# Kernel tuning notes

Measured on AMD Instinct MI355X. Metric: run time of the kernel, lower is better.

The kernel has to match this reference:

```python
import jax, jax.numpy as jnp
import numpy as np

N = 50000   # nodes
E = 800000  # edges
D = 128     # node_channels


def setup_inputs() -> dict:
    key = jax.random.key(0)
    ks = jax.random.split(key, 16)
    s = 1.0 / np.sqrt(D)
    inp = {
        "x": jax.random.normal(ks[0], (N, D), dtype=jnp.float32),
        "edge_index": jax.random.randint(ks[1], (2, E), 0, N, dtype=jnp.int64),
        "eps": jax.random.normal(ks[2], (N, D), dtype=jnp.float32),
    }
    names = ["1", "2", "mu", "logstd", "5", "6"]
    for i, nm in enumerate(names):
        inp[f"W{nm}"] = jax.random.normal(ks[3 + 2 * i], (D, D), dtype=jnp.float32) * s
        inp[f"b{nm}"] = jnp.zeros((D,), dtype=jnp.float32)
    return inp


def _gcn_norm(edge_index, num_nodes):
    # add self-loops, then symmetric normalization deg^{-1/2} (A+I) deg^{-1/2}
    loop = jnp.arange(num_nodes, dtype=edge_index.dtype)
    src = jnp.concatenate([edge_index[0], loop])
    dst = jnp.concatenate([edge_index[1], loop])
    deg = jax.ops.segment_sum(jnp.ones_like(src, dtype=jnp.float32), dst,
                              num_segments=num_nodes)
    dis = jnp.where(deg > 0, jax.lax.rsqrt(deg), 0.0)
    norm = dis[src] * dis[dst]  # [E + N]
    return src, dst, norm


def _gcn(x, W, b, src, dst, norm, num_nodes):
    h = x @ W                              # [N, D] small GEMM
    msg = h[src] * norm[:, None]           # gather + scale, [E+N, D]
    out = jax.ops.segment_sum(msg, dst, num_segments=num_nodes)  # scatter-add
    return out + b


def reference(x, edge_index, eps, W1, b1, W2, b2, Wmu, bmu, Wlogstd, blogstd,
              W5, b5, W6, b6):
    num_nodes = x.shape[0]
    src, dst, norm = _gcn_norm(edge_index, num_nodes)
    g = lambda h, W, b: _gcn(h, W, b, src, dst, norm, num_nodes)

    nodes = jax.nn.relu(g(x, W1, b1))
    nodes = jax.nn.relu(g(nodes, W2, b2))
    mu = g(nodes, Wmu, bmu)
    logstd = g(nodes, Wlogstd, blogstd)
    # reparametrize (training mode), divider = 10
    nodes = mu + eps * jnp.exp(logstd) / 10.0
    nodes = jax.nn.relu(g(nodes, W5, b5))
    nodes = jax.nn.relu(g(nodes, W6, b6))
    return nodes
```

## Files before the change

kernel.cpp:

```cpp
#include <hip/hip_runtime.h>
#include <hip/hip_bf16.h>
#include <cstdint>
#include <cstddef>

#define D 128
#define NWG 200

typedef _Float16 f16;
typedef f16 f16x2 __attribute__((ext_vector_type(2)));
typedef f16 f16x4 __attribute__((ext_vector_type(4)));
typedef f16 f16x8 __attribute__((ext_vector_type(8)));
typedef float f32x4 __attribute__((ext_vector_type(4)));

static inline size_t align256(size_t x){ return (x + 255) & ~(size_t)255; }

__global__ void detect_kernel(const int* __restrict__ ei, long long n32, int* __restrict__ flag){
  __shared__ int s;
  if (threadIdx.x == 0) s = 0;
  __syncthreads();
  int nz = 0;
  for (long long i = 2LL*threadIdx.x + 1; i < 4096 && i < n32; i += 512)
    nz |= (ei[i] != 0);
  if (nz) s = 1;
  __syncthreads();
  if (threadIdx.x == 0) *flag = (s ? 0 : 1);
}

__device__ __forceinline__ void load_edge(const void* ei, int E, int is64, int e, int& s, int& d){
  if (is64) {
    const long long* p = (const long long*)ei;
    s = (int)p[e]; d = (int)p[(size_t)E + e];
  } else {
    const int* p = (const int*)ei;
    s = p[e]; d = p[(size_t)E + e];
  }
}

__global__ __launch_bounds__(256) void passA_hist(
    const void* __restrict__ ei, int E, const int* __restrict__ flag,
    int* __restrict__ glob_hist, int NB){
  __shared__ int cnt[256];
  int t = threadIdx.x, wg = blockIdx.x;
  cnt[t] = 0;
  __syncthreads();
  int is64 = *flag;
  int chunk = (E + NWG - 1) / NWG;
  int lo = wg * chunk, hi = min(lo + chunk, E);
  for (int e = lo + t; e < hi; e += 256){
    int s, d;
    load_edge(ei, E, is64, e, s, d);
    atomicAdd(&cnt[d >> 8], 1);
  }
  __syncthreads();
  for (int b = t; b < NB; b += 256)
    glob_hist[b * NWG + wg] = cnt[b];
}

__global__ void scan_partial(const int* __restrict__ src, int* __restrict__ dst,
                             int* __restrict__ blockSums, int L){
  __shared__ int sd[256];
  int t = threadIdx.x;
  int base = blockIdx.x * 1024 + t * 4;
  int v[4]; int s = 0;
  #pragma unroll
  for (int j = 0; j < 4; ++j){ v[j] = (base + j < L) ? src[base + j] : 0; s += v[j]; }
  sd[t] = s; __syncthreads();
  for (int off = 1; off < 256; off <<= 1){
    int x = (t >= off) ? sd[t - off] : 0;
    __syncthreads();
    sd[t] += x;
    __syncthreads();
  }
  int run = sd[t] - s;
  #pragma unroll
  for (int j = 0; j < 4; ++j){
    if (base + j < L) dst[base + j] = run;
    run += v[j];
  }
  if (t == 255) blockSums[blockIdx.x] = sd[255];
}

__global__ void scan_blocksums(int* __restrict__ blockSums, int nblk,
                               int* __restrict__ dst, int L, int total){
  __shared__ int sd[256];
  int t = threadIdx.x;
  int v = (t < nblk) ? blockSums[t] : 0;
  sd[t] = v; __syncthreads();
  for (int off = 1; off < 256; off <<= 1){
    int x = (t >= off) ? sd[t - off] : 0;
    __syncthreads();
    sd[t] += x;
    __syncthreads();
  }
  if (t < nblk) blockSums[t] = sd[t] - v;
  if (t == 0) dst[L] = total;
}

__global__ void scan_add(int* __restrict__ dst, const int* __restrict__ blockSums, int L){
  int i = blockIdx.x * blockDim.x + threadIdx.x;
  if (i >= L) return;
  dst[i] += blockSums[i >> 10];
}

__global__ __launch_bounds__(256) void passB_scatter(
    const void* __restrict__ ei, int E, const int* __restrict__ flag,
    const int* __restrict__ bucketOff, int NB, unsigned* __restrict__ packed){
  __shared__ int cur[256];
  int t = threadIdx.x, wg = blockIdx.x;
  for (int b = t; b < NB; b += 256)
    cur[b] = bucketOff[b * NWG + wg];
  __syncthreads();
  int is64 = *flag;
  int chunk = (E + NWG - 1) / NWG;
  int lo = wg * chunk, hi = min(lo + chunk, E);
  for (int e = lo + t; e < hi; e += 256){
    int s, d;
    load_edge(ei, E, is64, e, s, d);
    int pos = atomicAdd(&cur[d >> 8], 1);
    packed[pos] = (unsigned)s | ((unsigned)(d & 255) << 16);
  }
}

__global__ __launch_bounds__(256) void passC_csr(
    const unsigned* __restrict__ packed, const int* __restrict__ bucketOff,
    int NB, int N, int E,
    int* __restrict__ rowptr, float* __restrict__ dis, int* __restrict__ csr_src){
  __shared__ int degl[256];
  __shared__ int sd[256];
  __shared__ int cur[256];
  int t = threadIdx.x, b = blockIdx.x;
  int begin = bucketOff[(size_t)b * NWG];
  int endb  = bucketOff[(size_t)(b + 1) * NWG];
  degl[t] = 0;
  __syncthreads();
  for (int i = begin + t; i < endb; i += 256)
    atomicAdd(&degl[(packed[i] >> 16) & 255], 1);
  __syncthreads();
  int dv = degl[t];
  sd[t] = dv; __syncthreads();
  for (int off = 1; off < 256; off <<= 1){
    int x = (t >= off) ? sd[t - off] : 0;
    __syncthreads();
    sd[t] += x;
    __syncthreads();
  }
  int localOff = sd[t] - dv;
  int v = b * 256 + t;
  if (v < N){
    rowptr[v] = begin + localOff;
    dis[v] = rsqrtf((float)(dv + 1));
  }
  if (b == NB - 1 && t == 0) rowptr[N] = E;
  cur[t] = begin + localOff;
  __syncthreads();
  for (int i = begin + t; i < endb; i += 256){
    unsigned p = packed[i];
    int pos = atomicAdd(&cur[(p >> 16) & 255], 1);
    csr_src[pos] = (int)(p & 0xFFFFu);
  }
}

__global__ void cast_scale(const float* __restrict__ in, const float* __restrict__ dis,
                           f16* __restrict__ out, int n4){
  int i = blockIdx.x * blockDim.x + threadIdx.x;
  if (i >= n4) return;
  float dv = dis[i >> 5];
  float4 v = ((const float4*)in)[i];
  f16x4 o; o[0]=(f16)(v.x*dv); o[1]=(f16)(v.y*dv); o[2]=(f16)(v.z*dv); o[3]=(f16)(v.w*dv);
  ((f16x4*)out)[i] = o;
}

__global__ void prep_w(const float* __restrict__ Wa, const float* __restrict__ Wb,
                       const float* __restrict__ Wc, const float* __restrict__ Wd,
                       const float* __restrict__ We, const float* __restrict__ Wf,
                       f16* __restrict__ Wt){
  int i = blockIdx.x * 256 + threadIdx.x;
  int w = i >> 14, rem = i & 16383;
  int n = rem >> 7, k = rem & 127;
  const float* Wp = (w==0)?Wa:(w==1)?Wb:(w==2)?Wc:(w==3)?Wd:(w==4)?We:Wf;
  Wt[i] = (f16)Wp[k*128 + n];
}

__global__ __launch_bounds__(256) void agg16(
    const f16* __restrict__ in, f16* __restrict__ out,
    const int* __restrict__ rowptr, const int* __restrict__ csr_src,
    const float* __restrict__ dis, int N){
  int v = blockIdx.x * 4 + (threadIdx.x >> 6);
  if (v >= N) return;
  int c2 = (threadIdx.x & 63) * 2;
  float dv = dis[v];
  int beg = rowptr[v], end = rowptr[v + 1];
  f16x2 sv = *(const f16x2*)&in[(size_t)v * D + c2];
  float acc0 = (float)sv[0], acc1 = (float)sv[1];
  int e = beg;
  for (; e + 7 < end; e += 8){
    f16x2 h[8];
    #pragma unroll
    for (int j = 0; j < 8; ++j){
      int u = csr_src[e + j];
      h[j] = *(const f16x2*)&in[(size_t)u * D + c2];
    }
    #pragma unroll
    for (int j = 0; j < 8; ++j){ acc0 += (float)h[j][0]; acc1 += (float)h[j][1]; }
  }
  for (; e + 1 < end; e += 2){
    int u0 = csr_src[e], u1 = csr_src[e + 1];
    f16x2 h0 = *(const f16x2*)&in[(size_t)u0 * D + c2];
    f16x2 h1 = *(const f16x2*)&in[(size_t)u1 * D + c2];
    acc0 += (float)h0[0] + (float)h1[0];
    acc1 += (float)h0[1] + (float)h1[1];
  }
  if (e < end){
    int u = csr_src[e];
    f16x2 h = *(const f16x2*)&in[(size_t)u * D + c2];
    acc0 += (float)h[0]; acc1 += (float)h[1];
  }
  f16x2 o; o[0] = (f16)(acc0 * dv); o[1] = (f16)(acc1 * dv);
  *(f16x2*)&out[(size_t)v * D + c2] = o;
}

template<int EPI>
__global__ __launch_bounds__(512) void gemm_mfma(
    const f16* __restrict__ A, const f16* __restrict__ Wt, const float* __restrict__ bias,
    const f16* __restrict__ Wt2, const float* __restrict__ bias2,
    const float* __restrict__ eps, const float* __restrict__ dis,
    f16* __restrict__ out16, float* __restrict__ outf, int N){

  extern __shared__ __align__(16) f16 Ws[];

  int t = threadIdx.x;
  int wave = t >> 6, lane = t & 63;
  int lrow = lane & 15, hi = lane >> 4;
  int r0 = blockIdx.x * 128 + wave * 16;
  bool active = (r0 < N);

  f16x8 a[4];
  if (active){
    int rr = min(r0 + lrow, N - 1);
    const f16* arow = &A[(size_t)rr * D + hi * 8];
    #pragma unroll
    for (int s = 0; s < 4; ++s) a[s] = *(const f16x8*)&arow[s * 32];
  }

  {
    int r = t & 127, p = t >> 7;
    const float4* src = (const float4*)&Wt[r * 128 + p * 32];
    f16* dstrow = &Ws[r * 128];
    #pragma unroll
    for (int i = 0; i < 4; ++i){
      int q = p * 4 + i;
      *(float4*)&dstrow[(q ^ (r & 7)) * 8] = src[i];
    }
    if (EPI == 1){
      const float4* src2 = (const float4*)&Wt2[r * 128 + p * 32];
      f16* dstrow2 = &Ws[16384 + r * 128];
      #pragma unroll
      for (int i = 0; i < 4; ++i){
        int q = p * 4 + i;
        *(float4*)&dstrow2[(q ^ (r & 7)) * 8] = src2[i];
      }
    }
  }
  __syncthreads();
  if (!active) return;

  f32x4 acc[8] = {};
  f32x4 acc2[8] = {};

  #pragma unroll
  for (int s = 0; s < 4; ++s){
    #pragma unroll
    for (int tt = 0; tt < 8; ++tt){
      int n = tt * 16 + lrow;
      int q = (s * 4 + hi) ^ (lrow & 7);
      f16x8 b = *(const f16x8*)&Ws[n * 128 + q * 8];
      acc[tt] = __builtin_amdgcn_mfma_f32_16x16x32_f16(b, a[s], acc[tt], 0, 0, 0);
      if (EPI == 1){
        f16x8 b2 = *(const f16x8*)&Ws[16384 + n * 128 + q * 8];
        acc2[tt] = __builtin_amdgcn_mfma_f32_16x16x32_f16(b2, a[s], acc2[tt], 0, 0, 0);
      }
    }
  }

  int r = r0 + lrow;
  if (r >= N) return;
  float dv = (EPI == 2) ? 1.f : dis[r];
  int cbase = hi * 4;
  #pragma unroll
  for (int tt = 0; tt < 8; ++tt){
    int n0 = tt * 16 + cbase;
    f32x4 bv = *(const f32x4*)&bias[n0];
    if (EPI == 0){
      f16x4 o;
      #pragma unroll
      for (int ii = 0; ii < 4; ++ii)
        o[ii] = (f16)(fmaxf(acc[tt][ii] + bv[ii], 0.f) * dv);
      *(f16x4*)&out16[(size_t)r * D + n0] = o;
    } else if (EPI == 1){
      f32x4 bv2 = *(const f32x4*)&bias2[n0];
      f32x4 e4  = *(const f32x4*)&eps[(size_t)r * D + n0];
      f16x4 o;
      #pragma unroll
      for (int ii = 0; ii < 4; ++ii){
        float mu = acc[tt][ii] + bv[ii];
        float ls = acc2[tt][ii] + bv2[ii];
        o[ii] = (f16)((mu + e4[ii] * __expf(ls) * 0.1f) * dv);
      }
      *(f16x4*)&out16[(size_t)r * D + n0] = o;
    } else {
      f32x4 o;
      #pragma unroll
      for (int ii = 0; ii < 4; ++ii)
        o[ii] = fmaxf(acc[tt][ii] + bv[ii], 0.f);
      *(f32x4*)&outf[(size_t)r * D + n0] = o;
    }
  }
}

extern "C" void kernel_launch(void* const* d_in, const int* in_sizes, int n_in,
                              void* d_out, int out_size, void* d_ws, size_t ws_size,
                              hipStream_t stream){
  const float* x   = (const float*)d_in[0];
  const void*  ei  = d_in[1];
  const float* eps = (const float*)d_in[2];
  const float* W1  = (const float*)d_in[3];  const float* b1  = (const float*)d_in[4];
  const float* W2  = (const float*)d_in[5];  const float* b2  = (const float*)d_in[6];
  const float* Wmu = (const float*)d_in[7];  const float* bmu = (const float*)d_in[8];
  const float* Wls = (const float*)d_in[9];  const float* bls = (const float*)d_in[10];
  const float* W5  = (const float*)d_in[11]; const float* b5  = (const float*)d_in[12];
  const float* W6  = (const float*)d_in[13]; const float* b6  = (const float*)d_in[14];

  const int N = in_sizes[0] / D;
  const int E = in_sizes[1] / 2;
  const int NB = (N + 255) >> 8;
  const int L  = NB * NWG;
  float* out = (float*)d_out;

  char* ws = (char*)d_ws;
  size_t off = 0;
  auto alloc = [&](size_t bytes){ char* p = ws + off; off += align256(bytes); return p; };
  int*      flag      = (int*)     alloc(256);
  int*      glob_hist = (int*)     alloc(((size_t)L + 1) * 4);
  int*      bucketOff = (int*)     alloc(((size_t)L + 1) * 4);
  int*      blockSums = (int*)     alloc(1024);
  int*      rowptr    = (int*)     alloc(((size_t)N + 1) * 4);
  float*    dis       = (float*)   alloc((size_t)N * 4);
  unsigned* packed    = (unsigned*)alloc((size_t)E * 4);
  int*      csr_src   = (int*)     alloc((size_t)E * 4);
  f16*      Wt        = (f16*)     alloc((size_t)6 * 128 * 128 * 2);
  f16*      bufA      = (f16*)     alloc((size_t)N * D * 2);
  f16*      bufB      = (f16*)     alloc((size_t)N * D * 2);
  (void)ws_size; (void)n_in; (void)out_size;

  detect_kernel<<<1, 256, 0, stream>>>((const int*)ei, (long long)2 * E, flag);

  passA_hist<<<NWG, 256, 0, stream>>>(ei, E, flag, glob_hist, NB);
  int nblk = (L + 1023) / 1024;
  scan_partial<<<nblk, 256, 0, stream>>>(glob_hist, bucketOff, blockSums, L);
  scan_blocksums<<<1, 256, 0, stream>>>(blockSums, nblk, bucketOff, L, E);
  scan_add<<<(L + 255) / 256, 256, 0, stream>>>(bucketOff, blockSums, L);
  passB_scatter<<<NWG, 256, 0, stream>>>(ei, E, flag, bucketOff, NB, packed);
  passC_csr<<<NB, 256, 0, stream>>>(packed, bucketOff, NB, N, E, rowptr, dis, csr_src);

  cast_scale<<<(N * D / 4 + 255) / 256, 256, 0, stream>>>(x, dis, bufB, N * D / 4);
  prep_w<<<(6 * 16384) / 256, 256, 0, stream>>>(W1, W2, Wmu, Wls, W5, W6, Wt);

  int aggGrid = (N + 3) / 4;
  int gemmGrid = (N + 127) / 128;
  size_t lds1 = 128 * 128 * sizeof(f16);
  size_t lds2 = 2 * 128 * 128 * sizeof(f16);

  agg16<<<aggGrid, 256, 0, stream>>>(bufB, bufA, rowptr, csr_src, dis, N);
  gemm_mfma<0><<<gemmGrid, 512, lds1, stream>>>(bufA, Wt + 0*16384, b1, nullptr, nullptr, nullptr, dis, bufB, nullptr, N);
  agg16<<<aggGrid, 256, 0, stream>>>(bufB, bufA, rowptr, csr_src, dis, N);
  gemm_mfma<0><<<gemmGrid, 512, lds1, stream>>>(bufA, Wt + 1*16384, b2, nullptr, nullptr, nullptr, dis, bufB, nullptr, N);
  agg16<<<aggGrid, 256, 0, stream>>>(bufB, bufA, rowptr, csr_src, dis, N);
  gemm_mfma<1><<<gemmGrid, 512, lds2, stream>>>(bufA, Wt + 2*16384, bmu, Wt + 3*16384, bls, eps, dis, bufB, nullptr, N);
  agg16<<<aggGrid, 256, 0, stream>>>(bufB, bufA, rowptr, csr_src, dis, N);
  gemm_mfma<0><<<gemmGrid, 512, lds1, stream>>>(bufA, Wt + 4*16384, b5, nullptr, nullptr, nullptr, dis, bufB, nullptr, N);
  agg16<<<aggGrid, 256, 0, stream>>>(bufB, bufA, rowptr, csr_src, dis, N);
  gemm_mfma<2><<<gemmGrid, 512, lds1, stream>>>(bufA, Wt + 5*16384, b6, nullptr, nullptr, nullptr, dis, nullptr, out, N);
}
```

Baseline: 396.6 us.

## Slice aggregation over feature columns and store CSR sources as 16-bit

The gather-aggregate kernel is split into four column passes of 32 channels each. Every node's 64-lane wave now processes four edges at once (16 lanes per edge) and combines the partial sums with cross-lane shuffles. Each pass touches a 64-byte slice of the feature rows, so its working set is a quarter of the node table, which is meant to improve L2/MALL hit rates on random gathers. CSR source indices are stored as u16 to halve index traffic, and index loads and output stores use nontemporal hints. The cost is four times as many blocks and four re-reads of the index arrays.

```diff
diff --git a/kernel.cpp b/kernel.cpp
--- a/kernel.cpp
+++ b/kernel.cpp
@@ -11,6 +11,7 @@
 typedef f16 f16x4 __attribute__((ext_vector_type(4)));
 typedef f16 f16x8 __attribute__((ext_vector_type(8)));
 typedef float f32x4 __attribute__((ext_vector_type(4)));
+typedef unsigned short u16;
 
 static inline size_t align256(size_t x){ return (x + 255) & ~(size_t)255; }
 
@@ -124,7 +125,7 @@
 __global__ __launch_bounds__(256) void passC_csr(
     const unsigned* __restrict__ packed, const int* __restrict__ bucketOff,
     int NB, int N, int E,
-    int* __restrict__ rowptr, float* __restrict__ dis, int* __restrict__ csr_src){
+    int* __restrict__ rowptr, float* __restrict__ dis, u16* __restrict__ csr_src){
   __shared__ int degl[256];
   __shared__ int sd[256];
   __shared__ int cur[256];
@@ -156,7 +157,7 @@
   for (int i = begin + t; i < endb; i += 256){
     unsigned p = packed[i];
     int pos = atomicAdd(&cur[(p >> 16) & 255], 1);
-    csr_src[pos] = (int)(p & 0xFFFFu);
+    csr_src[pos] = (u16)(p & 0xFFFFu);
   }
 }
 
@@ -181,42 +182,48 @@
   Wt[i] = (f16)Wp[k*128 + n];
 }
 
-__global__ __launch_bounds__(256) void agg16(
+__global__ __launch_bounds__(256) void agg_sliced(
     const f16* __restrict__ in, f16* __restrict__ out,
-    const int* __restrict__ rowptr, const int* __restrict__ csr_src,
-    const float* __restrict__ dis, int N){
-  int v = blockIdx.x * 4 + (threadIdx.x >> 6);
+    const int* __restrict__ rowptr, const u16* __restrict__ csr_src,
+    const float* __restrict__ dis, int N, int nodeBlocks){
+  int bid = blockIdx.x;
+  int pass = bid / nodeBlocks;
+  int nb   = bid - pass * nodeBlocks;
+  int v = nb * 4 + (threadIdx.x >> 6);
   if (v >= N) return;
-  int c2 = (threadIdx.x & 63) * 2;
-  float dv = dis[v];
+  int lane = threadIdx.x & 63;
+  int q  = lane >> 4;
+  int sl = lane & 15;
+  int c0 = pass * 32 + sl * 2;
+  const f16* base = in + c0;
+
   int beg = rowptr[v], end = rowptr[v + 1];
-  f16x2 sv = *(const f16x2*)&in[(size_t)v * D + c2];
-  float acc0 = (float)sv[0], acc1 = (float)sv[1];
-  int e = beg;
-  for (; e + 7 < end; e += 8){
-    f16x2 h[8];
-    #pragma unroll
-    for (int j = 0; j < 8; ++j){
-      int u = csr_src[e + j];
-      h[j] = *(const f16x2*)&in[(size_t)u * D + c2];
-    }
-    #pragma unroll
-    for (int j = 0; j < 8; ++j){ acc0 += (float)h[j][0]; acc1 += (float)h[j][1]; }
-  }
-  for (; e + 1 < end; e += 2){
-    int u0 = csr_src[e], u1 = csr_src[e + 1];
-    f16x2 h0 = *(const f16x2*)&in[(size_t)u0 * D + c2];
-    f16x2 h1 = *(const f16x2*)&in[(size_t)u1 * D + c2];
+  float acc0 = 0.f, acc1 = 0.f;
+  int e = beg + q;
+  for (; e + 4 < end; e += 8){
+    unsigned u0 = __builtin_nontemporal_load(&csr_src[e]);
+    unsigned u1 = __builtin_nontemporal_load(&csr_src[e + 4]);
+    f16x2 h0 = *(const f16x2*)&base[(size_t)u0 * D];
+    f16x2 h1 = *(const f16x2*)&base[(size_t)u1 * D];
     acc0 += (float)h0[0] + (float)h1[0];
     acc1 += (float)h0[1] + (float)h1[1];
   }
   if (e < end){
-    int u = csr_src[e];
-    f16x2 h = *(const f16x2*)&in[(size_t)u * D + c2];
+    unsigned u = __builtin_nontemporal_load(&csr_src[e]);
+    f16x2 h = *(const f16x2*)&base[(size_t)u * D];
     acc0 += (float)h[0]; acc1 += (float)h[1];
   }
-  f16x2 o; o[0] = (f16)(acc0 * dv); o[1] = (f16)(acc1 * dv);
-  *(f16x2*)&out[(size_t)v * D + c2] = o;
+  acc0 += __shfl_xor(acc0, 16); acc1 += __shfl_xor(acc1, 16);
+  acc0 += __shfl_xor(acc0, 32); acc1 += __shfl_xor(acc1, 32);
+
+  if (q == 0){
+    float dv = dis[v];
+    f16x2 sv = *(const f16x2*)&in[(size_t)v * D + c0];
+    f16x2 o;
+    o[0] = (f16)((acc0 + (float)sv[0]) * dv);
+    o[1] = (f16)((acc1 + (float)sv[1]) * dv);
+    __builtin_nontemporal_store(o, (f16x2*)&out[(size_t)v * D + c0]);
+  }
 }
 
 template<int EPI>
@@ -346,7 +353,7 @@
   int*      rowptr    = (int*)     alloc(((size_t)N + 1) * 4);
   float*    dis       = (float*)   alloc((size_t)N * 4);
   unsigned* packed    = (unsigned*)alloc((size_t)E * 4);
-  int*      csr_src   = (int*)     alloc((size_t)E * 4);
+  u16*      csr_src   = (u16*)     alloc((size_t)E * 2);
   f16*      Wt        = (f16*)     alloc((size_t)6 * 128 * 128 * 2);
   f16*      bufA      = (f16*)     alloc((size_t)N * D * 2);
   f16*      bufB      = (f16*)     alloc((size_t)N * D * 2);
@@ -365,19 +372,20 @@
   cast_scale<<<(N * D / 4 + 255) / 256, 256, 0, stream>>>(x, dis, bufB, N * D / 4);
   prep_w<<<(6 * 16384) / 256, 256, 0, stream>>>(W1, W2, Wmu, Wls, W5, W6, Wt);
 
-  int aggGrid = (N + 3) / 4;
+  int nodeBlocks = (N + 3) / 4;
+  int aggGrid = nodeBlocks * 4;
   int gemmGrid = (N + 127) / 128;
   size_t lds1 = 128 * 128 * sizeof(f16);
   size_t lds2 = 2 * 128 * 128 * sizeof(f16);
 
-  agg16<<<aggGrid, 256, 0, stream>>>(bufB, bufA, rowptr, csr_src, dis, N);
+  agg_sliced<<<aggGrid, 256, 0, stream>>>(bufB, bufA, rowptr, csr_src, dis, N, nodeBlocks);
   gemm_mfma<0><<<gemmGrid, 512, lds1, stream>>>(bufA, Wt + 0*16384, b1, nullptr, nullptr, nullptr, dis, bufB, nullptr, N);
-  agg16<<<aggGrid, 256, 0, stream>>>(bufB, bufA, rowptr, csr_src, dis, N);
+  agg_sliced<<<aggGrid, 256, 0, stream>>>(bufB, bufA, rowptr, csr_src, dis, N, nodeBlocks);
   gemm_mfma<0><<<gemmGrid, 512, lds1, stream>>>(bufA, Wt + 1*16384, b2, nullptr, nullptr, nullptr, dis, bufB, nullptr, N);
-  agg16<<<aggGrid, 256, 0, stream>>>(bufB, bufA, rowptr, csr_src, dis, N);
+  agg_sliced<<<aggGrid, 256, 0, stream>>>(bufB, bufA, rowptr, csr_src, dis, N, nodeBlocks);
   gemm_mfma<1><<<gemmGrid, 512, lds2, stream>>>(bufA, Wt + 2*16384, bmu, Wt + 3*16384, bls, eps, dis, bufB, nullptr, N);
-  agg16<<<aggGrid, 256, 0, stream>>>(bufB, bufA, rowptr, csr_src, dis, N);
+  agg_sliced<<<aggGrid, 256, 0, stream>>>(bufB, bufA, rowptr, csr_src, dis, N, nodeBlocks);
   gemm_mfma<0><<<gemmGrid, 512, lds1, stream>>>(bufA, Wt + 4*16384, b5, nullptr, nullptr, nullptr, dis, bufB, nullptr, N);
-  agg16<<<aggGrid, 256, 0, stream>>>(bufB, bufA, rowptr, csr_src, dis, N);
+  agg_sliced<<<aggGrid, 256, 0, stream>>>(bufB, bufA, rowptr, csr_src, dis, N, nodeBlocks);
   gemm_mfma<2><<<gemmGrid, 512, lds1, stream>>>(bufA, Wt + 5*16384, b6, nullptr, nullptr, nullptr, dis, nullptr, out, N);
 }
```

New measurement: 707.6 us. +78.4%, slower.
